# Optimization experiments

Measured on AMD Instinct MI355X. Metric: run time of the kernel, lower is better.

The kernel has to match this reference:

```python
import jax, jax.numpy as jnp
import numpy as np

N_NODES = 100000
N_EDGES = 1600000


def setup_inputs() -> dict:
    key = jax.random.key(0)
    k1, k2, k3, k4 = jax.random.split(key, 4)
    x = jax.random.normal(k1, (N_NODES, 256), dtype=jnp.float32)
    edge_index = jax.random.randint(k2, (2, N_EDGES), 0, N_NODES, dtype=jnp.int64)
    W1 = jax.random.normal(k3, (256, 128), dtype=jnp.float32) * (1.0 / np.sqrt(256))
    W2 = jax.random.normal(k4, (128, 40), dtype=jnp.float32) * (1.0 / np.sqrt(128))
    return {"x": x, "edge_index": edge_index, "W1": W1, "W2": W2}


def _gcn_conv(x, W, src, dst):
    # GCNConv(normalize=False, add_self_loops=False, bias=False):
    # linear transform then sum-aggregate messages along edges src->dst.
    h = x @ W                                   # [N, d_out]
    msg = h[src]                                # [E, d_out] gather
    return jax.ops.segment_sum(msg, dst, num_segments=N_NODES)  # [N, d_out] scatter-add


def reference(x, edge_index, W1, W2):
    src, dst = edge_index[0], edge_index[1]
    h = jax.nn.relu(_gcn_conv(x, W1, src, dst))
    # dropout is identity in eval mode
    out = _gcn_conv(h, W2, src, dst)
    return out
```

## Files before the change

kernel.cpp:

```cpp
#include <hip/hip_runtime.h>

constexpr int NN = 100000;
constexpr int NE = 1600000;
constexpr int DI = 256, DH = 128, DO = 40;

constexpr int NB = (NN + 255) >> 8;
constexpr int NB_BLK = 128;
constexpr int CHUNK = NE / NB_BLK;
constexpr int M2 = NB * NB_BLK;
constexpr int NBS = (M2 + 1023) / 1024;
constexpr int STAGE_CAP = 6144;

typedef __attribute__((ext_vector_type(8))) __bf16 bf16x8;
typedef __attribute__((ext_vector_type(4))) float f32x4;

__device__ inline float bf2f(__bf16 b) { return (float)b; }
__device__ inline float4 bf4_to_f4(ushort4 u) {
    return make_float4(__builtin_bit_cast(float, (unsigned)u.x << 16),
                       __builtin_bit_cast(float, (unsigned)u.y << 16),
                       __builtin_bit_cast(float, (unsigned)u.z << 16),
                       __builtin_bit_cast(float, (unsigned)u.w << 16));
}
__device__ inline unsigned short f2bf(float f) {
    return __builtin_bit_cast(unsigned short, (__bf16)f);
}
__device__ inline bf16x8 bf16x8_zero() {
    bf16x8 r;
    #pragma unroll
    for (int j = 0; j < 8; ++j) r[j] = (__bf16)0.f;
    return r;
}

__device__ inline bf16x8 load_cvt_a(const float* __restrict__ p, bool ok) {
    if (!ok) return bf16x8_zero();
    bf16x8 r;
    const float4 v0 = *(const float4*)p;
    const float4 v1 = *(const float4*)(p + 4);
    r[0] = (__bf16)v0.x; r[1] = (__bf16)v0.y; r[2] = (__bf16)v0.z; r[3] = (__bf16)v0.w;
    r[4] = (__bf16)v1.x; r[5] = (__bf16)v1.y; r[6] = (__bf16)v1.z; r[7] = (__bf16)v1.w;
    return r;
}

__global__ __launch_bounds__(256) void gemm1_kernel(const float* __restrict__ x,
                                                    const float* __restrict__ W,
                                                    __bf16* __restrict__ h1) {
    __shared__ __bf16 Wt[128][136];
    const int t = threadIdx.x;
    const int wave = t >> 6, lane = t & 63;
    const int q = lane >> 4, m = lane & 15;
    const int row0 = blockIdx.x * 128 + wave * 32;
    const int r0 = row0 + m, r1 = row0 + 16 + m;
    const bool ok0 = r0 < NN, ok1 = r1 < NN;
    const float* xp0 = x + (size_t)r0 * DI;
    const float* xp1 = x + (size_t)r1 * DI;
    const int sn = t & 127;
    const int kh = t >> 7;

    f32x4 acc[2][8];
    #pragma unroll
    for (int s = 0; s < 2; ++s)
        #pragma unroll
        for (int nt = 0; nt < 8; ++nt)
            #pragma unroll
            for (int rr = 0; rr < 4; ++rr) acc[s][nt][rr] = 0.f;

    for (int half = 0; half < 2; ++half) {
        const int kbase = half * 128;
        #pragma unroll 4
        for (int kl = kh * 64; kl < kh * 64 + 64; ++kl)
            Wt[sn][kl] = (__bf16)W[(size_t)(kbase + kl) * DH + sn];
        __syncthreads();
        #pragma unroll
        for (int kt = 0; kt < 4; ++kt) {
            const int lo = kt * 32 + q * 8;
            const bf16x8 a0 = load_cvt_a(xp0 + kbase + lo, ok0);
            const bf16x8 a1 = load_cvt_a(xp1 + kbase + lo, ok1);
            #pragma unroll
            for (int nt = 0; nt < 8; ++nt) {
                const bf16x8 b = *(const bf16x8*)(&Wt[nt * 16 + m][lo]);
                acc[0][nt] = __builtin_amdgcn_mfma_f32_16x16x32_bf16(a0, b, acc[0][nt], 0, 0, 0);
                acc[1][nt] = __builtin_amdgcn_mfma_f32_16x16x32_bf16(a1, b, acc[1][nt], 0, 0, 0);
            }
        }
        __syncthreads();
    }
    #pragma unroll
    for (int s = 0; s < 2; ++s)
        #pragma unroll
        for (int reg = 0; reg < 4; ++reg) {
            const int r = row0 + s * 16 + q * 4 + reg;
            if (r < NN) {
                __bf16* hp = h1 + (size_t)r * DH + m;
                #pragma unroll
                for (int nt = 0; nt < 8; ++nt) hp[nt * 16] = (__bf16)acc[s][nt][reg];
            }
        }
}

__global__ __launch_bounds__(256) void bucket_hist_kernel(const int* __restrict__ dst,
                                                          int* __restrict__ hist2d) {
    __shared__ int h[NB];
    for (int i = threadIdx.x; i < NB; i += 256) h[i] = 0;
    __syncthreads();
    const int base = blockIdx.x * CHUNK;
    for (int i = threadIdx.x; i < CHUNK; i += 256)
        atomicAdd(&h[dst[base + i] >> 8], 1);
    __syncthreads();
    for (int i = threadIdx.x; i < NB; i += 256)
        hist2d[i * NB_BLK + blockIdx.x] = h[i];
}

__global__ __launch_bounds__(256) void spart_kernel(const int* __restrict__ in,
                                                    int* __restrict__ bsum) {
    __shared__ int red[256];
    const int idx = blockIdx.x * 1024 + threadIdx.x * 4;
    int s = 0;
    if (idx < M2) { const int4 v = *(const int4*)(in + idx); s = v.x + v.y + v.z + v.w; }
    red[threadIdx.x] = s;
    __syncthreads();
    #pragma unroll
    for (int d = 128; d > 0; d >>= 1) {
        if (threadIdx.x < d) red[threadIdx.x] += red[threadIdx.x + d];
        __syncthreads();
    }
    if (threadIdx.x == 0) bsum[blockIdx.x] = red[0];
}

__global__ __launch_bounds__(64) void sblock_kernel(const int* __restrict__ bsum,
                                                    int* __restrict__ boff) {
    __shared__ int part[64];
    const int t = threadIdx.x;
    const int v = (t < NBS) ? bsum[t] : 0;
    part[t] = v;
    __syncthreads();
    for (int d = 1; d < 64; d <<= 1) {
        const int u = (t >= d) ? part[t - d] : 0;
        __syncthreads();
        part[t] += u;
        __syncthreads();
    }
    if (t < NBS) boff[t] = part[t] - v;
}

__global__ __launch_bounds__(256) void sfinal_kernel(const int* __restrict__ in,
                                                     const int* __restrict__ boff,
                                                     int* __restrict__ out) {
    __shared__ int part[256];
    const int t = threadIdx.x;
    const int idx = blockIdx.x * 1024 + t * 4;
    int4 v = make_int4(0, 0, 0, 0);
    if (idx < M2) v = *(const int4*)(in + idx);
    const int s = v.x + v.y + v.z + v.w;
    part[t] = s;
    __syncthreads();
    for (int d = 1; d < 256; d <<= 1) {
        const int u = (t >= d) ? part[t - d] : 0;
        __syncthreads();
        part[t] += u;
        __syncthreads();
    }
    if (idx < M2) {
        const int base = boff[blockIdx.x] + part[t] - s;
        *(int4*)(out + idx) = make_int4(base, base + v.x, base + v.x + v.y,
                                        base + v.x + v.y + v.z);
    }
}

__global__ __launch_bounds__(256) void bucket_scatter_kernel(const int* __restrict__ src,
                                                             const int* __restrict__ dst,
                                                             const int* __restrict__ offs2d,
                                                             int2* __restrict__ epair) {
    __shared__ int cur[NB];
    for (int i = threadIdx.x; i < NB; i += 256)
        cur[i] = offs2d[i * NB_BLK + blockIdx.x];
    __syncthreads();
    const int base = blockIdx.x * CHUNK;
    for (int i = threadIdx.x; i < CHUNK; i += 256) {
        const int d = dst[base + i], s = src[base + i];
        const int p = atomicAdd(&cur[d >> 8], 1);
        epair[p] = make_int2(s, d);
    }
}

__global__ __launch_bounds__(256) void bucket_sort_kernel(const int2* __restrict__ epair,
                                                          const int* __restrict__ offs2d,
                                                          int* __restrict__ off,
                                                          int* __restrict__ esrc) {
    __shared__ int cnt[256];
    __shared__ int incl[256];
    __shared__ int cur[256];
    __shared__ int stage[STAGE_CAP];
    const int b = blockIdx.x;
    const int t = threadIdx.x;
    const int bstart = offs2d[b * NB_BLK];
    const int bend = (b + 1 < NB) ? offs2d[(b + 1) * NB_BLK] : NE;
    const int n = bend - bstart;
    cnt[t] = 0;
    __syncthreads();
    for (int i = t; i < n; i += 256)
        atomicAdd(&cnt[epair[bstart + i].y & 255], 1);
    __syncthreads();
    incl[t] = cnt[t];
    __syncthreads();
    for (int d = 1; d < 256; d <<= 1) {
        const int u = (t >= d) ? incl[t - d] : 0;
        __syncthreads();
        incl[t] += u;
        __syncthreads();
    }
    const int ex = incl[t] - cnt[t];
    const int node = (b << 8) + t;
    if (node <= NN) off[node] = bstart + ex;
    cur[t] = ex;
    __syncthreads();
    const bool staged = (n <= STAGE_CAP);
    for (int i = t; i < n; i += 256) {
        const int2 pr = epair[bstart + i];
        const int p = atomicAdd(&cur[pr.y & 255], 1);
        if (staged) stage[p] = pr.x;
        else esrc[bstart + p] = pr.x;
    }
    __syncthreads();
    if (staged)
        for (int i = t; i < n; i += 256) esrc[bstart + i] = stage[i];
}

__global__ __launch_bounds__(256) void agg1_kernel(const __bf16* __restrict__ h1,
                                                   const int* __restrict__ esrc,
                                                   const int* __restrict__ off,
                                                   __bf16* __restrict__ agg) {
    const int w = (blockIdx.x * 256 + threadIdx.x) >> 6;
    if (w >= NN) return;
    const int lane = threadIdx.x & 63;
    const int half = lane >> 5;
    const int c = (lane & 31) * 4;
    const int b = off[w], e = off[w + 1];
    float4 a0 = make_float4(0.f, 0.f, 0.f, 0.f);
    float4 a1 = a0, a2 = a0, a3 = a0;
    int j = b + half;
    for (; j + 6 < e; j += 8) {
        const int s0 = esrc[j], s1 = esrc[j + 2], s2 = esrc[j + 4], s3 = esrc[j + 6];
        const float4 v0 = bf4_to_f4(*(const ushort4*)(h1 + (size_t)s0 * DH + c));
        const float4 v1 = bf4_to_f4(*(const ushort4*)(h1 + (size_t)s1 * DH + c));
        const float4 v2 = bf4_to_f4(*(const ushort4*)(h1 + (size_t)s2 * DH + c));
        const float4 v3 = bf4_to_f4(*(const ushort4*)(h1 + (size_t)s3 * DH + c));
        a0.x += v0.x; a0.y += v0.y; a0.z += v0.z; a0.w += v0.w;
        a1.x += v1.x; a1.y += v1.y; a1.z += v1.z; a1.w += v1.w;
        a2.x += v2.x; a2.y += v2.y; a2.z += v2.z; a2.w += v2.w;
        a3.x += v3.x; a3.y += v3.y; a3.z += v3.z; a3.w += v3.w;
    }
    for (; j < e; j += 2) {
        const int s = esrc[j];
        const float4 v = bf4_to_f4(*(const ushort4*)(h1 + (size_t)s * DH + c));
        a0.x += v.x; a0.y += v.y; a0.z += v.z; a0.w += v.w;
    }
    float4 acc = make_float4(a0.x + a1.x + a2.x + a3.x,
                             a0.y + a1.y + a2.y + a3.y,
                             a0.z + a1.z + a2.z + a3.z,
                             a0.w + a1.w + a2.w + a3.w);
    acc.x += __shfl_xor(acc.x, 32);
    acc.y += __shfl_xor(acc.y, 32);
    acc.z += __shfl_xor(acc.z, 32);
    acc.w += __shfl_xor(acc.w, 32);
    if (half == 0) {
        ushort4 o;
        o.x = f2bf(fmaxf(acc.x, 0.f));
        o.y = f2bf(fmaxf(acc.y, 0.f));
        o.z = f2bf(fmaxf(acc.z, 0.f));
        o.w = f2bf(fmaxf(acc.w, 0.f));
        *(ushort4*)(agg + (size_t)w * DH + c) = o;
    }
}

__global__ __launch_bounds__(256) void gemm2_kernel(const __bf16* __restrict__ agg,
                                                    const float* __restrict__ W2,
                                                    __bf16* __restrict__ h2) {
    __shared__ __bf16 Wt2[48][136];
    const int t = threadIdx.x;
    const int wave = t >> 6, lane = t & 63;
    const int q = lane >> 4, m = lane & 15;
    const int row0 = blockIdx.x * 64 + wave * 16;
    for (int i = t; i < DH * DO; i += 256) {
        const int k = i / DO, n = i % DO;
        Wt2[n][k] = (__bf16)W2[i];
    }
    for (int i = t; i < 8 * DH; i += 256)
        Wt2[DO + (i >> 7)][i & 127] = (__bf16)0.f;
    __syncthreads();
    const int r = row0 + m;
    const bool okA = r < NN;
    const __bf16* ap = agg + (size_t)r * DH;
    f32x4 acc[3];
    #pragma unroll
    for (int nt = 0; nt < 3; ++nt)
        #pragma unroll
        for (int rr = 0; rr < 4; ++rr) acc[nt][rr] = 0.f;
    #pragma unroll
    for (int ks = 0; ks < 4; ++ks) {
        const int k0 = ks * 32 + q * 8;
        const bf16x8 a = okA ? *(const bf16x8*)(ap + k0) : bf16x8_zero();
        #pragma unroll
        for (int nt = 0; nt < 3; ++nt) {
            const bf16x8 b = *(const bf16x8*)(&Wt2[nt * 16 + m][k0]);
            acc[nt] = __builtin_amdgcn_mfma_f32_16x16x32_bf16(a, b, acc[nt], 0, 0, 0);
        }
    }
    #pragma unroll
    for (int reg = 0; reg < 4; ++reg) {
        const int rr = row0 + q * 4 + reg;
        if (rr < NN) {
            #pragma unroll
            for (int nt = 0; nt < 3; ++nt) {
                const int cc = nt * 16 + m;
                if (cc < DO) h2[(size_t)rr * DO + cc] = (__bf16)acc[nt][reg];
            }
        }
    }
}

__global__ __launch_bounds__(256) void agg2_kernel(const __bf16* __restrict__ h2,
                                                   const int* __restrict__ esrc,
                                                   const int* __restrict__ off,
                                                   float* __restrict__ out) {
    const int w = (blockIdx.x * 256 + threadIdx.x) >> 6;
    if (w >= NN) return;
    const int lane = threadIdx.x & 63;
    const int sub = lane / 10;
    const int c = (lane % 10) * 4;
    const int b = off[w], e = off[w + 1];
    float4 a0 = make_float4(0.f, 0.f, 0.f, 0.f);
    float4 a1 = a0, a2 = a0;
    if (sub < 6) {
        int j = b + sub;
        for (; j + 12 < e; j += 18) {
            const int s0 = esrc[j], s1 = esrc[j + 6], s2 = esrc[j + 12];
            const float4 v0 = bf4_to_f4(*(const ushort4*)(h2 + (size_t)s0 * DO + c));
            const float4 v1 = bf4_to_f4(*(const ushort4*)(h2 + (size_t)s1 * DO + c));
            const float4 v2 = bf4_to_f4(*(const ushort4*)(h2 + (size_t)s2 * DO + c));
            a0.x += v0.x; a0.y += v0.y; a0.z += v0.z; a0.w += v0.w;
            a1.x += v1.x; a1.y += v1.y; a1.z += v1.z; a1.w += v1.w;
            a2.x += v2.x; a2.y += v2.y; a2.z += v2.z; a2.w += v2.w;
        }
        for (; j < e; j += 6) {
            const int s = esrc[j];
            const float4 v = bf4_to_f4(*(const ushort4*)(h2 + (size_t)s * DO + c));
            a0.x += v.x; a0.y += v.y; a0.z += v.z; a0.w += v.w;
        }
    }
    float4 acc = make_float4(a0.x + a1.x + a2.x, a0.y + a1.y + a2.y,
                             a0.z + a1.z + a2.z, a0.w + a1.w + a2.w);
    acc.x += __shfl(acc.x, lane + 30);
    acc.y += __shfl(acc.y, lane + 30);
    acc.z += __shfl(acc.z, lane + 30);
    acc.w += __shfl(acc.w, lane + 30);
    const float ax = acc.x + __shfl(acc.x, lane + 10) + __shfl(acc.x, lane + 20);
    const float ay = acc.y + __shfl(acc.y, lane + 10) + __shfl(acc.y, lane + 20);
    const float az = acc.z + __shfl(acc.z, lane + 10) + __shfl(acc.z, lane + 20);
    const float aw = acc.w + __shfl(acc.w, lane + 10) + __shfl(acc.w, lane + 20);
    if (lane < 10) {
        *(float4*)(out + (size_t)w * DO + c) = make_float4(ax, ay, az, aw);
    }
}

extern "C" void kernel_launch(void* const* d_in, const int* in_sizes, int n_in,
                              void* d_out, int out_size, void* d_ws, size_t ws_size,
                              hipStream_t stream) {
    const float* x  = (const float*)d_in[0];
    const int*   ei = (const int*)d_in[1];
    const float* W1 = (const float*)d_in[2];
    const float* W2 = (const float*)d_in[3];
    const int* src = ei;
    const int* dst = ei + NE;

    __bf16* h1  = (__bf16*)d_ws;
    __bf16* agg = h1 + (size_t)NN * DH;
    __bf16* h2  = h1;
    int2* epair = (int2*)(agg + (size_t)NN * DH);
    int* ints   = (int*)(epair + NE);
    int* esrc   = ints;
    int* off    = esrc + NE;
    int* hist2d = off + NN + 1;
    int* offs2d = hist2d + M2;
    int* bsum   = offs2d + M2;
    int* boff   = bsum + NBS;

    float* out = (float*)d_out;

    gemm1_kernel<<<(NN + 127) / 128, 256, 0, stream>>>(x, W1, h1);
    bucket_hist_kernel<<<NB_BLK, 256, 0, stream>>>(dst, hist2d);
    spart_kernel<<<NBS, 256, 0, stream>>>(hist2d, bsum);
    sblock_kernel<<<1, 64, 0, stream>>>(bsum, boff);
    sfinal_kernel<<<NBS, 256, 0, stream>>>(hist2d, boff, offs2d);
    bucket_scatter_kernel<<<NB_BLK, 256, 0, stream>>>(src, dst, offs2d, epair);
    bucket_sort_kernel<<<NB, 256, 0, stream>>>(epair, offs2d, off, esrc);
    agg1_kernel<<<(NN * 64 + 255) / 256, 256, 0, stream>>>(h1, esrc, off, agg);
    gemm2_kernel<<<(NN + 63) / 64, 256, 0, stream>>>(agg, W2, h2);
    agg2_kernel<<<(NN * 64 + 255) / 256, 256, 0, stream>>>(h2, esrc, off, out);
}
```

Measured before the change: 375.5 us.

## Prepack W1 into MFMA fragment layout and pack edge pairs into 32-bit words

Adds a small kernel that converts W1 to bf16 once, laid out in MFMA B-fragment order. gemm1 then reads its fragments straight from global/L2 instead of having every block transpose W1 into shared memory with barriers. gemm1 now processes 64 rows per block with one 16-row tile per wave, preloading all A fragments. Separately, the bucket scatter/sort now store src plus the low 8 bits of dst in a single 32-bit word instead of an int2, halving that intermediate traffic; this relies on node ids fitting in 24 bits.

```diff
diff --git a/kernel.cpp b/kernel.cpp
--- a/kernel.cpp
+++ b/kernel.cpp
@@ -30,7 +30,6 @@
     for (int j = 0; j < 8; ++j) r[j] = (__bf16)0.f;
     return r;
 }
-
 __device__ inline bf16x8 load_cvt_a(const float* __restrict__ p, bool ok) {
     if (!ok) return bf16x8_zero();
     bf16x8 r;
@@ -41,60 +40,58 @@
     return r;
 }
 
+__global__ __launch_bounds__(256) void w1pack_kernel(const float* __restrict__ W,
+                                                     __bf16* __restrict__ Wf) {
+    const int i = blockIdx.x * 256 + threadIdx.x;
+    const int j = i & 7;
+    const int lane = (i >> 3) & 63;
+    const int nt = (i >> 9) & 7;
+    const int kt = i >> 12;
+    const int k = kt * 32 + (lane >> 4) * 8 + j;
+    const int n = nt * 16 + (lane & 15);
+    Wf[i] = (__bf16)W[(size_t)k * DH + n];
+}
+
 __global__ __launch_bounds__(256) void gemm1_kernel(const float* __restrict__ x,
-                                                    const float* __restrict__ W,
+                                                    const __bf16* __restrict__ Wf,
                                                     __bf16* __restrict__ h1) {
-    __shared__ __bf16 Wt[128][136];
     const int t = threadIdx.x;
     const int wave = t >> 6, lane = t & 63;
     const int q = lane >> 4, m = lane & 15;
-    const int row0 = blockIdx.x * 128 + wave * 32;
-    const int r0 = row0 + m, r1 = row0 + 16 + m;
-    const bool ok0 = r0 < NN, ok1 = r1 < NN;
-    const float* xp0 = x + (size_t)r0 * DI;
-    const float* xp1 = x + (size_t)r1 * DI;
-    const int sn = t & 127;
-    const int kh = t >> 7;
-
-    f32x4 acc[2][8];
-    #pragma unroll
-    for (int s = 0; s < 2; ++s)
+    const int row0 = blockIdx.x * 64 + wave * 16;
+    const int r = row0 + m;
+    const bool ok = r < NN;
+    const float* xp = x + (size_t)r * DI;
+
+    bf16x8 a[8];
+    #pragma unroll
+    for (int kt = 0; kt < 8; ++kt)
+        a[kt] = load_cvt_a(xp + kt * 32 + q * 8, ok);
+
+    f32x4 acc[8];
+    #pragma unroll
+    for (int nt = 0; nt < 8; ++nt)
         #pragma unroll
-        for (int nt = 0; nt < 8; ++nt)
+        for (int rr = 0; rr < 4; ++rr) acc[nt][rr] = 0.f;
+
+    const bf16x8* wf = (const bf16x8*)Wf;
+    #pragma unroll
+    for (int kt = 0; kt < 8; ++kt) {
+        #pragma unroll
+        for (int nt = 0; nt < 8; ++nt) {
+            const bf16x8 b = wf[(kt * 8 + nt) * 64 + lane];
+            acc[nt] = __builtin_amdgcn_mfma_f32_16x16x32_bf16(a[kt], b, acc[nt], 0, 0, 0);
+        }
+    }
+    #pragma unroll
+    for (int reg = 0; reg < 4; ++reg) {
+        const int rr = row0 + q * 4 + reg;
+        if (rr < NN) {
+            __bf16* hp = h1 + (size_t)rr * DH + m;
             #pragma unroll
-            for (int rr = 0; rr < 4; ++rr) acc[s][nt][rr] = 0.f;
-
-    for (int half = 0; half < 2; ++half) {
-        const int kbase = half * 128;
-        #pragma unroll 4
-        for (int kl = kh * 64; kl < kh * 64 + 64; ++kl)
-            Wt[sn][kl] = (__bf16)W[(size_t)(kbase + kl) * DH + sn];
-        __syncthreads();
-        #pragma unroll
-        for (int kt = 0; kt < 4; ++kt) {
-            const int lo = kt * 32 + q * 8;
-            const bf16x8 a0 = load_cvt_a(xp0 + kbase + lo, ok0);
-            const bf16x8 a1 = load_cvt_a(xp1 + kbase + lo, ok1);
-            #pragma unroll
-            for (int nt = 0; nt < 8; ++nt) {
-                const bf16x8 b = *(const bf16x8*)(&Wt[nt * 16 + m][lo]);
-                acc[0][nt] = __builtin_amdgcn_mfma_f32_16x16x32_bf16(a0, b, acc[0][nt], 0, 0, 0);
-                acc[1][nt] = __builtin_amdgcn_mfma_f32_16x16x32_bf16(a1, b, acc[1][nt], 0, 0, 0);
-            }
-        }
-        __syncthreads();
-    }
-    #pragma unroll
-    for (int s = 0; s < 2; ++s)
-        #pragma unroll
-        for (int reg = 0; reg < 4; ++reg) {
-            const int r = row0 + s * 16 + q * 4 + reg;
-            if (r < NN) {
-                __bf16* hp = h1 + (size_t)r * DH + m;
-                #pragma unroll
-                for (int nt = 0; nt < 8; ++nt) hp[nt * 16] = (__bf16)acc[s][nt][reg];
-            }
-        }
+            for (int nt = 0; nt < 8; ++nt) hp[nt * 16] = (__bf16)acc[nt][reg];
+        }
+    }
 }
 
 __global__ __launch_bounds__(256) void bucket_hist_kernel(const int* __restrict__ dst,
@@ -169,7 +166,7 @@
 __global__ __launch_bounds__(256) void bucket_scatter_kernel(const int* __restrict__ src,
                                                              const int* __restrict__ dst,
                                                              const int* __restrict__ offs2d,
-                                                             int2* __restrict__ epair) {
+                                                             unsigned* __restrict__ epack) {
     __shared__ int cur[NB];
     for (int i = threadIdx.x; i < NB; i += 256)
         cur[i] = offs2d[i * NB_BLK + blockIdx.x];
@@ -178,11 +175,11 @@
     for (int i = threadIdx.x; i < CHUNK; i += 256) {
         const int d = dst[base + i], s = src[base + i];
         const int p = atomicAdd(&cur[d >> 8], 1);
-        epair[p] = make_int2(s, d);
-    }
-}
-
-__global__ __launch_bounds__(256) void bucket_sort_kernel(const int2* __restrict__ epair,
+        epack[p] = (unsigned)s | ((unsigned)(d & 255) << 24);
+    }
+}
+
+__global__ __launch_bounds__(256) void bucket_sort_kernel(const unsigned* __restrict__ epack,
                                                           const int* __restrict__ offs2d,
                                                           int* __restrict__ off,
                                                           int* __restrict__ esrc) {
@@ -198,7 +195,7 @@
     cnt[t] = 0;
     __syncthreads();
     for (int i = t; i < n; i += 256)
-        atomicAdd(&cnt[epair[bstart + i].y & 255], 1);
+        atomicAdd(&cnt[epack[bstart + i] >> 24], 1);
     __syncthreads();
     incl[t] = cnt[t];
     __syncthreads();
@@ -215,10 +212,11 @@
     __syncthreads();
     const bool staged = (n <= STAGE_CAP);
     for (int i = t; i < n; i += 256) {
-        const int2 pr = epair[bstart + i];
-        const int p = atomicAdd(&cur[pr.y & 255], 1);
-        if (staged) stage[p] = pr.x;
-        else esrc[bstart + p] = pr.x;
+        const unsigned pk = epack[bstart + i];
+        const int p = atomicAdd(&cur[pk >> 24], 1);
+        const int s = (int)(pk & 0xFFFFFFu);
+        if (staged) stage[p] = s;
+        else esrc[bstart + p] = s;
     }
     __syncthreads();
     if (staged)
@@ -372,11 +370,12 @@
     const int* src = ei;
     const int* dst = ei + NE;
 
-    __bf16* h1  = (__bf16*)d_ws;
+    __bf16* Wf  = (__bf16*)d_ws;
+    __bf16* h1  = Wf + 32768;
     __bf16* agg = h1 + (size_t)NN * DH;
     __bf16* h2  = h1;
-    int2* epair = (int2*)(agg + (size_t)NN * DH);
-    int* ints   = (int*)(epair + NE);
+    unsigned* epack = (unsigned*)(agg + (size_t)NN * DH);
+    int* ints   = (int*)(epack + NE);
     int* esrc   = ints;
     int* off    = esrc + NE;
     int* hist2d = off + NN + 1;
@@ -386,13 +385,14 @@
 
     float* out = (float*)d_out;
 
-    gemm1_kernel<<<(NN + 127) / 128, 256, 0, stream>>>(x, W1, h1);
+    w1pack_kernel<<<128, 256, 0, stream>>>(W1, Wf);
+    gemm1_kernel<<<(NN + 63) / 64, 256, 0, stream>>>(x, Wf, h1);
     bucket_hist_kernel<<<NB_BLK, 256, 0, stream>>>(dst, hist2d);
     spart_kernel<<<NBS, 256, 0, stream>>>(hist2d, bsum);
     sblock_kernel<<<1, 64, 0, stream>>>(bsum, boff);
     sfinal_kernel<<<NBS, 256, 0, stream>>>(hist2d, boff, offs2d);
-    bucket_scatter_kernel<<<NB_BLK, 256, 0, stream>>>(src, dst, offs2d, epair);
-    bucket_sort_kernel<<<NB, 256, 0, stream>>>(epair, offs2d, off, esrc);
+    bucket_scatter_kernel<<<NB_BLK, 256, 0, stream>>>(src, dst, offs2d, epack);
+    bucket_sort_kernel<<<NB, 256, 0, stream>>>(epack, offs2d, off, esrc);
     agg1_kernel<<<(NN * 64 + 255) / 256, 256, 0, stream>>>(h1, esrc, off, agg);
     gemm2_kernel<<<(NN + 63) / 64, 256, 0, stream>>>(agg, W2, h2);
     agg2_kernel<<<(NN * 64 + 255) / 256, 256, 0, stream>>>(h2, esrc, off, out);
```

Result: faster. 366.7 us (-2.3%).
